# Kernel optimization log

Measured on AMD Instinct MI355X. Metric: run time of the kernel, lower is better.

The kernel has to match this reference:

```python
import jax, jax.numpy as jnp
import numpy as np

B, L, H = 4096, 512, 32  # batch, latent_dim, hidden_size


def setup_inputs() -> dict:
    key = jax.random.key(0)
    ks = jax.random.split(key, 8)
    mu = jax.random.normal(ks[0], (B, L), jnp.float32)
    log_var = jax.random.normal(ks[1], (B, L), jnp.float32)
    eps0 = jax.random.normal(ks[2], (B,), jnp.float32)
    eps = jax.random.normal(ks[3], (B, L), jnp.float32)
    # Per-step MiniSampler params. Sampler idx has in_size = idx+1.
    # Zero-pad first-layer weights to [L, H, L]; row idx only uses cols 0..idx.
    mask = (jnp.arange(L)[None, :] <= jnp.arange(L)[:, None]).astype(jnp.float32)  # [L, L]
    W1 = jax.random.normal(ks[4], (L, H, L), jnp.float32) * 0.1 * mask[:, None, :]
    b1 = jax.random.normal(ks[5], (L, H), jnp.float32) * 0.1
    W2 = jax.random.normal(ks[6], (L, 2, H), jnp.float32) * 0.1
    b2 = jax.random.normal(ks[7], (L, 2), jnp.float32) * 0.1
    return {"mu": mu, "log_var": log_var, "eps0": eps0, "eps": eps,
            "W1": W1, "b1": b1, "W2": W2, "b2": b2}


def reference(mu, log_var, eps0, eps, W1, b1, W2, b2):
    # sample=False path (the default). First latent is reparameterized:
    std0 = jnp.exp(0.5 * log_var[:, 0])
    input0 = eps0 * std0 + mu[:, 0]                      # [B]
    # Input to sampler idx is [input0, mu[:,0], ..., mu[:,idx-1]];
    # W1 is column-masked so one shared padded vector works for all steps.
    v = jnp.concatenate([input0[:, None], mu[:, :-1]], axis=1)  # [B, L]
    h = jax.nn.leaky_relu(jnp.einsum('bj,ihj->bih', v, W1) + b1[None])  # [B, L, H]
    out = jnp.einsum('bih,ioh->bio', h, W2) + b2[None]   # [B, L, 2]
    mus_resampled = out[..., 0]                          # [B, L]
    log_vars_resampled = out[..., 1]                     # [B, L]
    samples = eps * jnp.exp(0.5 * log_vars_resampled) + mus_resampled  # [B, L]
    return (mus_resampled, log_vars_resampled, samples)
```

## Files before the change

kernel.cpp:

```cpp
#include <hip/hip_runtime.h>
#include <hip/hip_bf16.h>

#define Bn 4096
#define Ln 512
#define Hn 32
#define MT 4

using bf16x8 = __attribute__((ext_vector_type(8))) __bf16;
using f32x4  = __attribute__((ext_vector_type(4))) float;

#define GLOAD_LDS16(g, l)                                                          \
  __builtin_amdgcn_global_load_lds(                                                \
      (const __attribute__((address_space(1))) void*)(g),                          \
      (__attribute__((address_space(3))) void*)(l), 16, 0, 0)

__device__ __forceinline__ unsigned short f2bf(float x) {
  unsigned int u = __float_as_uint(x);
  unsigned int r = (u + 0x7FFFu + ((u >> 16) & 1u)) >> 16;
  return (unsigned short)r;
}

__global__ __launch_bounds__(256) void prep_w1_kernel(const float* __restrict__ W1,
                                                      unsigned short* __restrict__ W1b) {
  int idx = blockIdx.x * 256 + threadIdx.x;
  const int n  = idx >> 7;
  const int c0 = (idx & 127) * 4;
  const int i  = n >> 5;
  if (c0 > i) return;
  const float4 f = reinterpret_cast<const float4*>(W1)[idx];
  ushort4 o;
  o.x = f2bf(f.x); o.y = f2bf(f.y); o.z = f2bf(f.z); o.w = f2bf(f.w);
  reinterpret_cast<ushort4*>(W1b)[idx] = o;
}

__global__ __launch_bounds__(256) void prep_v_kernel(const float* __restrict__ mu,
                                                     const float* __restrict__ log_var,
                                                     const float* __restrict__ eps0,
                                                     unsigned short* __restrict__ Vb) {
  int idx = blockIdx.x * 256 + threadIdx.x;
  int b = idx >> 9, j = idx & 511;
  float v;
  if (j == 0) {
    v = eps0[b] * expf(0.5f * log_var[(size_t)b * Ln]) + mu[(size_t)b * Ln];
  } else {
    v = mu[(size_t)b * Ln + j - 1];
  }
  Vb[idx] = f2bf(v);
}

__global__ __launch_bounds__(256) void gemm_fused_kernel(
    const unsigned short* __restrict__ Vb,
    const unsigned short* __restrict__ W1b,
    const float* __restrict__ b1,
    const float* __restrict__ W2,
    const float* __restrict__ b2,
    const float* __restrict__ eps,
    float* __restrict__ out)
{
  const int tid  = threadIdx.x;
  const int wid  = tid >> 6;
  const int lane = tid & 63;
  const int l15  = lane & 15;
  const int lq   = lane >> 4;

  const int bid = blockIdx.x;
  const int xcd = bid & 7;
  const int s   = bid >> 3;
  const int bn  = xcd + 8 * (15 - (s >> 3));
  const int mg  = s & 7;
  const int mb  = mg * (MT * 128);
  const int nb  = bn * 128;

  const int ksteps = min(8, (bn + 16) >> 4);

  __shared__ unsigned short As[2 * 128 * 64];
  __shared__ unsigned short Bs[2 * 128 * 64];

  const int rowc = lane >> 3;
  const int sswz = (lane & 7) ^ rowc;
  const unsigned short* gA = Vb  + (size_t)(mb + wid * 32 + rowc) * Ln + sswz * 8;
  const unsigned short* gB = W1b + (size_t)(nb + wid * 32 + rowc) * Ln + sswz * 8;
  unsigned short* lA = As + wid * 2048;
  unsigned short* lB = Bs + wid * 2048;

  auto STAGE = [&](int buf, int mt, int k0e) {
    const int    lofs = buf * 8192;
    const size_t ga   = (size_t)mt * (128 * Ln) + k0e;
#pragma unroll
    for (int j = 0; j < 4; ++j) {
      GLOAD_LDS16(gA + ga + (size_t)j * 8 * Ln, lA + lofs + j * 512);
      GLOAD_LDS16(gB + k0e + (size_t)j * 8 * Ln, lB + lofs + j * 512);
    }
  };

  const int arow = (wid >> 1) * 64 + l15;
  const int brow = (wid & 1) * 64 + l15;
  const int swz7 = l15 & 7;

  float4 b1q[2][2], w20q[2][2], w21q[2][2];
  float  bias0[2], bias1[2];
#pragma unroll
  for (int il = 0; il < 2; ++il) {
    const int i = bn * 4 + (wid & 1) * 2 + il;
#pragma unroll
    for (int q = 0; q < 2; ++q) {
      const int hb = q * 16 + lq * 4;
      b1q[il][q]  = *reinterpret_cast<const float4*>(b1 + i * Hn + hb);
      w20q[il][q] = *reinterpret_cast<const float4*>(W2 + (i * 2 + 0) * Hn + hb);
      w21q[il][q] = *reinterpret_cast<const float4*>(W2 + (i * 2 + 1) * Hn + hb);
    }
    bias0[il] = b2[i * 2 + 0];
    bias1[il] = b2[i * 2 + 1];
  }

  f32x4 acc[4][4];
#pragma unroll
  for (int fn = 0; fn < 4; ++fn)
#pragma unroll
    for (int fm = 0; fm < 4; ++fm) acc[fn][fm] = f32x4{0.f, 0.f, 0.f, 0.f};

  auto COMPUTE = [&](int buf) {
    const int cofs = buf * 8192;
#pragma unroll
    for (int ks2 = 0; ks2 < 2; ++ks2) {
      const int se = ((ks2 * 4 + lq) ^ swz7) * 8;
      bf16x8 a[4], b[4];
#pragma unroll
      for (int f = 0; f < 4; ++f) {
        a[f] = *reinterpret_cast<const bf16x8*>(As + cofs + (arow + f * 16) * 64 + se);
        b[f] = *reinterpret_cast<const bf16x8*>(Bs + cofs + (brow + f * 16) * 64 + se);
      }
#pragma unroll
      for (int fn = 0; fn < 4; ++fn)
#pragma unroll
        for (int fm = 0; fm < 4; ++fm)
          acc[fn][fm] = __builtin_amdgcn_mfma_f32_16x16x32_bf16(b[fn], a[fm], acc[fn][fm], 0, 0, 0);
    }
  };

  float* mus = out;
  float* lvs = out + (size_t)Bn * Ln;
  float* smp = out + (size_t)2 * Bn * Ln;

  int buf = 0;
  STAGE(0, 0, 0);

  for (int mt = 0; mt < MT; ++mt) {
    for (int k = 0; k < ksteps; ++k) {
      int kn = k + 1, mtn = mt;
      if (kn == ksteps) { kn = 0; ++mtn; }
      if (mtn < MT) {
        STAGE(buf ^ 1, mtn, kn * 64);
        asm volatile("s_waitcnt vmcnt(8)" ::: "memory");
      } else {
        asm volatile("s_waitcnt vmcnt(0)" ::: "memory");
      }
      __builtin_amdgcn_s_barrier();
      __builtin_amdgcn_sched_barrier(0);
      COMPUTE(buf);

      if (k == ksteps - 1) {
        float* S = reinterpret_cast<float*>(Bs + buf * 8192);
        __builtin_amdgcn_s_barrier();

        const int wrow = (wid >> 1) * 64;
#pragma unroll
        for (int il = 0; il < 2; ++il) {
          const int icl = (wid & 1) * 2 + il;
#pragma unroll
          for (int fm = 0; fm < 4; ++fm) {
            float p0 = 0.f, p1 = 0.f;
#pragma unroll
            for (int q = 0; q < 2; ++q) {
              const f32x4& A = acc[il * 2 + q][fm];
              const float* b1f = reinterpret_cast<const float*>(&b1q[il][q]);
              const float* w0f = reinterpret_cast<const float*>(&w20q[il][q]);
              const float* w1f = reinterpret_cast<const float*>(&w21q[il][q]);
#pragma unroll
              for (int r = 0; r < 4; ++r) {
                float x  = A[r] + b1f[r];
                float hv = fmaxf(x, 0.01f * x);
                p0 += hv * w0f[r];
                p1 += hv * w1f[r];
              }
            }
            p0 += __shfl_xor(p0, 16);
            p0 += __shfl_xor(p0, 32);
            p1 += __shfl_xor(p1, 16);
            p1 += __shfl_xor(p1, 32);
            if (lq == 0) {
              const int r = wrow + fm * 16 + l15;
              S[icl * 128 + r]       = p0 + bias0[il];
              S[512 + icl * 128 + r] = p1 + bias1[il];
            }
          }
        }
        asm volatile("s_waitcnt lgkmcnt(0)" ::: "memory");
        __builtin_amdgcn_s_barrier();

        if (tid < 128) {
          const int    r = tid;
          const size_t o = (size_t)(mb + mt * 128 + r) * Ln + bn * 4;
          float4 muv, lvv;
          muv.x = S[r];       muv.y = S[128 + r]; muv.z = S[256 + r]; muv.w = S[384 + r];
          lvv.x = S[512 + r]; lvv.y = S[640 + r]; lvv.z = S[768 + r]; lvv.w = S[896 + r];
          const float4 ep = *reinterpret_cast<const float4*>(eps + o);
          float4 sm;
          sm.x = ep.x * __builtin_exp2f(lvv.x * 0.7213475204444817f) + muv.x;
          sm.y = ep.y * __builtin_exp2f(lvv.y * 0.7213475204444817f) + muv.y;
          sm.z = ep.z * __builtin_exp2f(lvv.z * 0.7213475204444817f) + muv.z;
          sm.w = ep.w * __builtin_exp2f(lvv.w * 0.7213475204444817f) + muv.w;
          *reinterpret_cast<float4*>(mus + o) = muv;
          *reinterpret_cast<float4*>(lvs + o) = lvv;
          *reinterpret_cast<float4*>(smp + o) = sm;
        }
#pragma unroll
        for (int fn = 0; fn < 4; ++fn)
#pragma unroll
          for (int fm = 0; fm < 4; ++fm) acc[fn][fm] = f32x4{0.f, 0.f, 0.f, 0.f};
      }
      __builtin_amdgcn_s_barrier();
      buf ^= 1;
    }
  }
}

extern "C" void kernel_launch(void* const* d_in, const int* in_sizes, int n_in,
                              void* d_out, int out_size, void* d_ws, size_t ws_size,
                              hipStream_t stream) {
  const float* mu      = (const float*)d_in[0];
  const float* log_var = (const float*)d_in[1];
  const float* eps0    = (const float*)d_in[2];
  const float* eps     = (const float*)d_in[3];
  const float* W1      = (const float*)d_in[4];
  const float* b1      = (const float*)d_in[5];
  const float* W2      = (const float*)d_in[6];
  const float* b2      = (const float*)d_in[7];
  float* out = (float*)d_out;

  unsigned short* Vb  = (unsigned short*)d_ws;
  unsigned short* W1b = (unsigned short*)((char*)d_ws + (size_t)Bn * Ln * 2);

  prep_v_kernel<<<(Bn * Ln) / 256, 256, 0, stream>>>(mu, log_var, eps0, Vb);
  prep_w1_kernel<<<(Ln * Hn * Ln) / 4 / 256, 256, 0, stream>>>(W1, W1b);
  gemm_fused_kernel<<<128 * (32 / MT), 256, 0, stream>>>(
      Vb, W1b, b1, W2, b2, eps, out);
}
```

Before: 79.99 us.

## Prefetch epilogue operands alongside staging and write outputs directly without LDS

Moves the b1/W2/b2 and eps loads into the epilogue iteration, issued before the next tile's staging loads, with tuned vmcnt waits so they overlap the last k-step's compute. The epilogue now writes mu, log_var and samples straight from lanes to global memory instead of gathering through LDS with extra barriers. It also regroups the block-to-column-tile mapping and makes prep_w1 write zeros into the masked region. The tradeoff is scattered scalar stores and fragile hand-counted vmcnt values that depend on the exact number of outstanding loads.

After: 95.40 us. +19.3%, slower.

```diff
diff --git a/kernel.cpp b/kernel.cpp
--- a/kernel.cpp
+++ b/kernel.cpp
@@ -26,10 +26,13 @@
   const int n  = idx >> 7;
   const int c0 = (idx & 127) * 4;
   const int i  = n >> 5;
-  if (c0 > i) return;
-  const float4 f = reinterpret_cast<const float4*>(W1)[idx];
   ushort4 o;
-  o.x = f2bf(f.x); o.y = f2bf(f.y); o.z = f2bf(f.z); o.w = f2bf(f.w);
+  if (c0 > i) {
+    o.x = 0; o.y = 0; o.z = 0; o.w = 0;
+  } else {
+    const float4 f = reinterpret_cast<const float4*>(W1)[idx];
+    o.x = f2bf(f.x); o.y = f2bf(f.y); o.z = f2bf(f.z); o.w = f2bf(f.w);
+  }
   reinterpret_cast<ushort4*>(W1b)[idx] = o;
 }
 
@@ -63,13 +66,14 @@
   const int l15  = lane & 15;
   const int lq   = lane >> 4;
 
-  const int bid = blockIdx.x;
-  const int xcd = bid & 7;
-  const int s   = bid >> 3;
-  const int bn  = xcd + 8 * (15 - (s >> 3));
-  const int mg  = s & 7;
-  const int mb  = mg * (MT * 128);
-  const int nb  = bn * 128;
+  const int bid  = blockIdx.x;
+  const int xcd  = bid & 7;
+  const int s    = bid >> 3;
+  const int g    = xcd + 8 * (3 - (s >> 5));
+  const int bn   = g * 4 + ((s >> 3) & 3);
+  const int mg   = s & 7;
+  const int mb   = mg * (MT * 128);
+  const int nb   = bn * 128;
 
   const int ksteps = min(8, (bn + 16) >> 4);
 
@@ -83,9 +87,9 @@
   unsigned short* lA = As + wid * 2048;
   unsigned short* lB = Bs + wid * 2048;
 
-  auto STAGE = [&](int buf, int mt, int k0e) {
-    const int    lofs = buf * 8192;
-    const size_t ga   = (size_t)mt * (128 * Ln) + k0e;
+  auto STAGE = [&](int bufw, int mt_, int k0e) {
+    const int    lofs = bufw * 8192;
+    const size_t ga   = (size_t)mt_ * (128 * Ln) + k0e;
 #pragma unroll
     for (int j = 0; j < 4; ++j) {
       GLOAD_LDS16(gA + ga + (size_t)j * 8 * Ln, lA + lofs + j * 512);
@@ -97,30 +101,14 @@
   const int brow = (wid & 1) * 64 + l15;
   const int swz7 = l15 & 7;
 
-  float4 b1q[2][2], w20q[2][2], w21q[2][2];
-  float  bias0[2], bias1[2];
-#pragma unroll
-  for (int il = 0; il < 2; ++il) {
-    const int i = bn * 4 + (wid & 1) * 2 + il;
-#pragma unroll
-    for (int q = 0; q < 2; ++q) {
-      const int hb = q * 16 + lq * 4;
-      b1q[il][q]  = *reinterpret_cast<const float4*>(b1 + i * Hn + hb);
-      w20q[il][q] = *reinterpret_cast<const float4*>(W2 + (i * 2 + 0) * Hn + hb);
-      w21q[il][q] = *reinterpret_cast<const float4*>(W2 + (i * 2 + 1) * Hn + hb);
-    }
-    bias0[il] = b2[i * 2 + 0];
-    bias1[il] = b2[i * 2 + 1];
-  }
-
   f32x4 acc[4][4];
 #pragma unroll
   for (int fn = 0; fn < 4; ++fn)
 #pragma unroll
     for (int fm = 0; fm < 4; ++fm) acc[fn][fm] = f32x4{0.f, 0.f, 0.f, 0.f};
 
-  auto COMPUTE = [&](int buf) {
-    const int cofs = buf * 8192;
+  auto COMPUTE = [&](int bufc) {
+    const int cofs = bufc * 8192;
 #pragma unroll
     for (int ks2 = 0; ks2 < 2; ++ks2) {
       const int se = ((ks2 * 4 + lq) ^ swz7) * 8;
@@ -134,7 +122,9 @@
       for (int fn = 0; fn < 4; ++fn)
 #pragma unroll
         for (int fm = 0; fm < 4; ++fm)
-          acc[fn][fm] = __builtin_amdgcn_mfma_f32_16x16x32_bf16(b[fn], a[fm], acc[fn][fm], 0, 0, 0);
+          acc[fn][fm] = __builtin_amdgcn_mfma_f32_16x16x32_bf16(b[fn], a[ks2 ? fm : fm],
+                                                                acc[fn][fm], 0, 0, 0),
+          (void)0;
     }
   };
 
@@ -149,24 +139,53 @@
     for (int k = 0; k < ksteps; ++k) {
       int kn = k + 1, mtn = mt;
       if (kn == ksteps) { kn = 0; ++mtn; }
-      if (mtn < MT) {
+      const bool epi  = (k == ksteps - 1);
+      const bool more = (mtn < MT);
+
+      float2 ep2[4];
+      float4 b1q[2][2], w20q[2][2], w21q[2][2], b2q;
+      if (epi) {
+        int zero;
+        asm volatile("v_mov_b32 %0, 0" : "=v"(zero));
+        const int    wrow = (wid >> 1) * 64;
+        const size_t er   = (size_t)(mb + mt * 128 + wrow + l15);
+        const int    ec   = bn * 4 + (wid & 1) * 2;
+#pragma unroll
+        for (int fm = 0; fm < 4; ++fm)
+          ep2[fm] = *reinterpret_cast<const float2*>(eps + (er + fm * 16) * Ln + ec + zero);
+#pragma unroll
+        for (int il = 0; il < 2; ++il) {
+          const int i = bn * 4 + (wid & 1) * 2 + il;
+#pragma unroll
+          for (int q = 0; q < 2; ++q) {
+            const int hb = q * 16 + lq * 4 + zero;
+            b1q[il][q]  = *reinterpret_cast<const float4*>(b1 + i * Hn + hb);
+            w20q[il][q] = *reinterpret_cast<const float4*>(W2 + (i * 2 + 0) * Hn + hb);
+            w21q[il][q] = *reinterpret_cast<const float4*>(W2 + (i * 2 + 1) * Hn + hb);
+          }
+        }
+        b2q = *reinterpret_cast<const float4*>(b2 + (bn * 4 + (wid & 1) * 2) * 2 + zero);
+        __builtin_amdgcn_sched_barrier(0);
+      }
+
+      if (more) {
         STAGE(buf ^ 1, mtn, kn * 64);
-        asm volatile("s_waitcnt vmcnt(8)" ::: "memory");
+        if (epi) asm volatile("s_waitcnt vmcnt(25)" ::: "memory");
+        else     asm volatile("s_waitcnt vmcnt(8)"  ::: "memory");
       } else {
-        asm volatile("s_waitcnt vmcnt(0)" ::: "memory");
+        asm volatile("s_waitcnt vmcnt(17)" ::: "memory");
       }
       __builtin_amdgcn_s_barrier();
       __builtin_amdgcn_sched_barrier(0);
       COMPUTE(buf);
 
-      if (k == ksteps - 1) {
-        float* S = reinterpret_cast<float*>(Bs + buf * 8192);
-        __builtin_amdgcn_s_barrier();
-
+      if (epi) {
         const int wrow = (wid >> 1) * 64;
 #pragma unroll
         for (int il = 0; il < 2; ++il) {
-          const int icl = (wid & 1) * 2 + il;
+          const int   icl   = (wid & 1) * 2 + il;
+          const float bias0 = (il == 0) ? b2q.x : b2q.z;
+          const float bias1 = (il == 0) ? b2q.y : b2q.w;
 #pragma unroll
           for (int fm = 0; fm < 4; ++fm) {
             float p0 = 0.f, p1 = 0.f;
@@ -189,30 +208,16 @@
             p1 += __shfl_xor(p1, 16);
             p1 += __shfl_xor(p1, 32);
             if (lq == 0) {
-              const int r = wrow + fm * 16 + l15;
-              S[icl * 128 + r]       = p0 + bias0[il];
-              S[512 + icl * 128 + r] = p1 + bias1[il];
+              const size_t o = (size_t)(mb + mt * 128 + wrow + fm * 16 + l15) * Ln
+                               + bn * 4 + icl;
+              const float mu_o = p0 + bias0;
+              const float lv_o = p1 + bias1;
+              const float ep   = (il == 0) ? ep2[fm].x : ep2[fm].y;
+              mus[o] = mu_o;
+              lvs[o] = lv_o;
+              smp[o] = ep * __builtin_exp2f(lv_o * 0.7213475204444817f) + mu_o;
             }
           }
-        }
-        asm volatile("s_waitcnt lgkmcnt(0)" ::: "memory");
-        __builtin_amdgcn_s_barrier();
-
-        if (tid < 128) {
-          const int    r = tid;
-          const size_t o = (size_t)(mb + mt * 128 + r) * Ln + bn * 4;
-          float4 muv, lvv;
-          muv.x = S[r];       muv.y = S[128 + r]; muv.z = S[256 + r]; muv.w = S[384 + r];
-          lvv.x = S[512 + r]; lvv.y = S[640 + r]; lvv.z = S[768 + r]; lvv.w = S[896 + r];
-          const float4 ep = *reinterpret_cast<const float4*>(eps + o);
-          float4 sm;
-          sm.x = ep.x * __builtin_exp2f(lvv.x * 0.7213475204444817f) + muv.x;
-          sm.y = ep.y * __builtin_exp2f(lvv.y * 0.7213475204444817f) + muv.y;
-          sm.z = ep.z * __builtin_exp2f(lvv.z * 0.7213475204444817f) + muv.z;
-          sm.w = ep.w * __builtin_exp2f(lvv.w * 0.7213475204444817f) + muv.w;
-          *reinterpret_cast<float4*>(mus + o) = muv;
-          *reinterpret_cast<float4*>(lvs + o) = lvv;
-          *reinterpret_cast<float4*>(smp + o) = sm;
         }
 #pragma unroll
         for (int fn = 0; fn < 4; ++fn)
```
